# Optimization experiments

Measured on AMD Instinct MI355X. Metric: run time of the kernel, lower is better.

The kernel has to match this reference:

```python
import jax, jax.numpy as jnp
import numpy as np

LN_EPS = 1e-5


def setup_inputs() -> dict:
    key = jax.random.key(0)
    k1, k2 = jax.random.split(key, 2)
    B, C, D, H, W = 2, 96, 32, 128, 128
    out_dim = 2 * C
    x = jax.random.normal(k1, (B, C, D, H, W), dtype=jnp.float32)
    # nn.Linear(8*C, out_dim, bias=False): weight shape (out_dim, 8*C)
    w = jax.random.normal(k2, (out_dim, 8 * C), dtype=jnp.float32) * 0.02
    gamma = jnp.ones((8 * C,), dtype=jnp.float32)
    beta = jnp.zeros((8 * C,), dtype=jnp.float32)
    return {"x": x, "w": w, "gamma": gamma, "beta": beta}


def reference(x, w, gamma, beta):
    B, C, D, H, W = x.shape
    D2, H2, W2 = D // 2, H // 2, W // 2
    # Strided 2x2x2 gather: reshape then move (dd,hh,ww) offsets next to C.
    # torch.cat order [x0..x7] = (dd,hh,ww) lexicographic, dd most significant,
    # with C channels per block -> layout (..., dd, hh, ww, C) flattened.
    xr = x.reshape(B, C, D2, 2, H2, 2, W2, 2)
    xr = xr.transpose(0, 2, 4, 6, 3, 5, 7, 1)  # (B, D2, H2, W2, dd, hh, ww, C)
    xf = xr.reshape(B, D2, H2, W2, 8 * C)
    # LayerNorm over last dim
    mu = jnp.mean(xf, axis=-1, keepdims=True)
    xc = xf - mu
    var = jnp.mean(xc * xc, axis=-1, keepdims=True)
    xn = xc * jax.lax.rsqrt(var + LN_EPS) * gamma + beta
    # Linear (no bias): y = xn @ w.T
    y = jnp.einsum('bdhwc,oc->bdhwo', xn, w)
    # back to channels-first (B, out_dim, D2, H2, W2)
    return y.transpose(0, 4, 1, 2, 3)
```

## Files before the change

kernel.cpp:

```cpp
#include <hip/hip_runtime.h>
#include <hip/hip_bf16.h>

typedef __attribute__((ext_vector_type(8))) short short8;
typedef __attribute__((ext_vector_type(4))) float f32x4;

#define LN_EPS 1e-5f

__device__ __forceinline__ unsigned short f2bf(float f) {
  union { float f; unsigned u; } v; v.f = f;
  unsigned r = v.u + 0x7FFFu + ((v.u >> 16) & 1u);
  return (unsigned short)(r >> 16);
}

__device__ __forceinline__ int a_addr(int row, int colb) {
  return row * 1536 + (colb ^ ((row & 7) << 4));
}


__global__ __launch_bounds__(256) void pm_prep(
    const float* __restrict__ w, const float* __restrict__ g,
    const float* __restrict__ be, unsigned short* __restrict__ wg,
    float* __restrict__ sb) {
  const int o = blockIdx.x;
  const int t = threadIdx.x;
  const int lane = t & 63, wv = t >> 6;
  __shared__ float red[4][2];
  float sa = 0.f, ba = 0.f;
#pragma unroll
  for (int u = 0; u < 3; ++u) {
    int kp = t + 256 * u;
    int dh = kp / 192;
    int rem = kp - dh * 192;
    int c = rem >> 1, ww = rem & 1;
    int k = dh * 192 + ww * 96 + c;
    float wv_ = w[o * 768 + k];
    float v = wv_ * g[k];
    sa += v;
    ba += wv_ * be[k];
    int NT = o >> 4, ks = kp >> 5, qq = (kp >> 3) & 3, jj = kp & 7;
    wg[(((NT * 24 + ks) * 64) + qq * 16 + (o & 15)) * 8 + jj] = f2bf(v);
  }
#pragma unroll
  for (int d = 1; d < 64; d <<= 1) {
    sa += __shfl_xor(sa, d);
    ba += __shfl_xor(ba, d);
  }
  if (lane == 0) { red[wv][0] = sa; red[wv][1] = ba; }
  __syncthreads();
  if (t == 0) {
    sb[o] = red[0][0] + red[1][0] + red[2][0] + red[3][0];
    sb[192 + o] = red[0][1] + red[1][1] + red[2][1] + red[3][1];
  }
}

__global__ __launch_bounds__(256, 3) void pm_main(
    const float* __restrict__ x, const unsigned short* __restrict__ wg,
    const float* __restrict__ sb, float* __restrict__ out) {
  const int bid = blockIdx.x;
  const int wh = bid & 1;
  const int h2 = (bid >> 1) & 63;
  const int d2 = (bid >> 7) & 15;
  const int b = bid >> 11;
  const int t = threadIdx.x;
  const int lane = t & 63, wv = t >> 6;
  const int q = lane & 15, sc = lane >> 4;

  __shared__ __align__(16) unsigned char A_lds[32 * 1536];
  __shared__ float part[4][32][2];
  __shared__ float stats[32][2];

  const float* xb = x + (size_t)b * (96 * 32 * 128 * 128);
  const int cp0 = wv * 12 + sc * 3;
  const float* pc[3];
#pragma unroll
  for (int i = 0; i < 3; ++i)
    pc[i] = xb + (size_t)(2 * (cp0 + i)) * 524288 + wh * 64 + 4 * q;

  float sum0 = 0.f, sq0 = 0.f, sum1 = 0.f, sq1 = 0.f;
  float4 xa[2][3], xc[2][3];

  auto issue = [&](int p, int buf) {
    int off = (2 * d2 + (p >> 1)) * 16384 + (2 * h2 + (p & 1)) * 128;
#pragma unroll
    for (int i = 0; i < 3; ++i) {
      xa[buf][i] = *(const float4*)(pc[i] + off);
      xc[buf][i] = *(const float4*)(pc[i] + 524288 + off);
    }
  };

  auto consume = [&](int p, int buf) {
#pragma unroll
    for (int i = 0; i < 3; ++i) {
      float4 f0 = xa[buf][i], f1 = xc[buf][i];
      sum0 += (f0.x + f0.y) + (f1.x + f1.y);
      sq0  += f0.x * f0.x + f0.y * f0.y + f1.x * f1.x + f1.y * f1.y;
      sum1 += (f0.z + f0.w) + (f1.z + f1.w);
      sq1  += f0.z * f0.z + f0.w * f0.w + f1.z * f1.z + f1.w * f1.w;
      int colb = p * 384 + 8 * (cp0 + i);
      *(ushort4*)&A_lds[a_addr(2 * q, colb)] =
          make_ushort4(f2bf(f0.x), f2bf(f0.y), f2bf(f1.x), f2bf(f1.y));
      *(ushort4*)&A_lds[a_addr(2 * q + 1, colb)] =
          make_ushort4(f2bf(f0.z), f2bf(f0.w), f2bf(f1.z), f2bf(f1.w));
    }
  };

  const int al = lane & 15, ah = lane >> 4;
  const short8* wgs = (const short8*)wg;
  f32x4 acc[2][3];
#pragma unroll
  for (int mt = 0; mt < 2; ++mt)
#pragma unroll
    for (int nt = 0; nt < 3; ++nt) acc[mt][nt] = {0.f, 0.f, 0.f, 0.f};

  issue(0, 0);
  issue(1, 1);

#pragma unroll
  for (int p = 0; p < 4; ++p) {
    const int buf = p & 1;
    consume(p, buf);
    if (p == 3) {
      sum0 += __shfl_xor(sum0, 16); sum0 += __shfl_xor(sum0, 32);
      sq0  += __shfl_xor(sq0, 16);  sq0  += __shfl_xor(sq0, 32);
      sum1 += __shfl_xor(sum1, 16); sum1 += __shfl_xor(sum1, 32);
      sq1  += __shfl_xor(sq1, 16);  sq1  += __shfl_xor(sq1, 32);
      if (sc == 0) {
        part[wv][2 * q][0] = sum0;     part[wv][2 * q][1] = sq0;
        part[wv][2 * q + 1][0] = sum1; part[wv][2 * q + 1][1] = sq1;
      }
    }
    __syncthreads();

    short8 bfr[6][3];
#pragma unroll
    for (int ksi = 0; ksi < 6; ++ksi)
#pragma unroll
      for (int nt = 0; nt < 3; ++nt)
        bfr[ksi][nt] = wgs[((wv * 3 + nt) * 24 + (p * 6 + ksi)) * 64 + lane];

    if (p < 2) issue(p + 2, buf);

    if (p == 3) {
      int row = t & 31;
      float S = part[0][row][0] + part[1][row][0] + part[2][row][0] + part[3][row][0];
      float Q = part[0][row][1] + part[1][row][1] + part[2][row][1] + part[3][row][1];
      float mu = S * (1.f / 768.f);
      float var = Q * (1.f / 768.f) - mu * mu;
      float rs = rsqrtf(var + LN_EPS);
      stats[row][0] = rs;
      stats[row][1] = mu * rs;
    }

#pragma unroll
    for (int ksi = 0; ksi < 6; ++ksi) {
      int ks = p * 6 + ksi;
      short8 afr[2];
#pragma unroll
      for (int mt = 0; mt < 2; ++mt)
        afr[mt] = *(const short8*)&A_lds[a_addr(mt * 16 + al, ks * 64 + ah * 16)];
#pragma unroll
      for (int nt = 0; nt < 3; ++nt)
#pragma unroll
        for (int mt = 0; mt < 2; ++mt)
          acc[mt][nt] = __builtin_amdgcn_mfma_f32_16x16x32_bf16(afr[mt], bfr[ksi][nt], acc[mt][nt], 0, 0, 0);
    }
  }
  __syncthreads();

#pragma unroll
  for (int nt = 0; nt < 3; ++nt) {
    int o = wv * 48 + nt * 16 + al;
    float Sv = sb[o], Bv = sb[192 + o];
    float* ob = out + (((size_t)(b * 192 + o) * 16 + d2) * 64 + h2) * 64 + wh * 32;
#pragma unroll
    for (int mt = 0; mt < 2; ++mt) {
      int m0 = mt * 16 + ah * 4;
      float4 y;
      y.x = stats[m0 + 0][0] * acc[mt][nt][0] - stats[m0 + 0][1] * Sv + Bv;
      y.y = stats[m0 + 1][0] * acc[mt][nt][1] - stats[m0 + 1][1] * Sv + Bv;
      y.z = stats[m0 + 2][0] * acc[mt][nt][2] - stats[m0 + 2][1] * Sv + Bv;
      y.w = stats[m0 + 3][0] * acc[mt][nt][3] - stats[m0 + 3][1] * Sv + Bv;
      *(float4*)(ob + m0) = y;
    }
  }
}

extern "C" void kernel_launch(void* const* d_in, const int* in_sizes, int n_in,
                              void* d_out, int out_size, void* d_ws, size_t ws_size,
                              hipStream_t stream) {
  (void)in_sizes; (void)n_in; (void)out_size; (void)ws_size;
  const float* x  = (const float*)d_in[0];
  const float* w  = (const float*)d_in[1];
  const float* g  = (const float*)d_in[2];
  const float* be = (const float*)d_in[3];
  unsigned short* wg = (unsigned short*)d_ws;
  float* sb = (float*)((char*)d_ws + 192 * 768 * sizeof(unsigned short));
  pm_prep<<<192, 256, 0, stream>>>(w, g, be, wg, sb);
  pm_main<<<4096, 256, 0, stream>>>(x, wg, sb, (float*)d_out);
}
```

Measured before the change: 163.0 us.

## Make main kernel persistent over four tiles with cross-tile prefetch

Each block now processes four consecutive 32-row tiles instead of one, cutting the grid from 4096 to 1024 blocks. The prefetch pipeline is reduced to a single buffer but now crosses tile boundaries, so the next tile's first slice loads while the current epilogue and MFMA work run. This amortizes block launch and setup and keeps loads in flight between tiles. In exchange the grid is smaller, which may lower occupancy and load balance across CUs, and the prefetch depth drops from two stages to one.

```diff
diff --git a/kernel.cpp b/kernel.cpp
--- a/kernel.cpp
+++ b/kernel.cpp
@@ -57,10 +57,9 @@
     const float* __restrict__ x, const unsigned short* __restrict__ wg,
     const float* __restrict__ sb, float* __restrict__ out) {
   const int bid = blockIdx.x;
-  const int wh = bid & 1;
-  const int h2 = (bid >> 1) & 63;
-  const int d2 = (bid >> 7) & 15;
-  const int b = bid >> 11;
+  const int h2g = bid & 31;
+  const int d2 = (bid >> 5) & 15;
+  const int b = bid >> 9;
   const int t = threadIdx.x;
   const int lane = t & 63, wv = t >> 6;
   const int q = lane & 15, sc = lane >> 4;
@@ -74,24 +73,26 @@
   const float* pc[3];
 #pragma unroll
   for (int i = 0; i < 3; ++i)
-    pc[i] = xb + (size_t)(2 * (cp0 + i)) * 524288 + wh * 64 + 4 * q;
-
-  float sum0 = 0.f, sq0 = 0.f, sum1 = 0.f, sq1 = 0.f;
-  float4 xa[2][3], xc[2][3];
-
-  auto issue = [&](int p, int buf) {
-    int off = (2 * d2 + (p >> 1)) * 16384 + (2 * h2 + (p & 1)) * 128;
+    pc[i] = xb + (size_t)(2 * (cp0 + i)) * 524288 + 4 * q;
+
+  float sum0, sq0, sum1, sq1;
+  float4 xa[3], xc[3];
+
+  auto issue = [&](int tt, int p) {
+    int wh = tt & 1;
+    int h2 = 2 * h2g + (tt >> 1);
+    int off = (2 * d2 + (p >> 1)) * 16384 + (2 * h2 + (p & 1)) * 128 + wh * 64;
 #pragma unroll
     for (int i = 0; i < 3; ++i) {
-      xa[buf][i] = *(const float4*)(pc[i] + off);
-      xc[buf][i] = *(const float4*)(pc[i] + 524288 + off);
+      xa[i] = *(const float4*)(pc[i] + off);
+      xc[i] = *(const float4*)(pc[i] + 524288 + off);
     }
   };
 
-  auto consume = [&](int p, int buf) {
+  auto consume = [&](int p) {
 #pragma unroll
     for (int i = 0; i < 3; ++i) {
-      float4 f0 = xa[buf][i], f1 = xc[buf][i];
+      float4 f0 = xa[i], f1 = xc[i];
       sum0 += (f0.x + f0.y) + (f1.x + f1.y);
       sq0  += f0.x * f0.x + f0.y * f0.y + f1.x * f1.x + f1.y * f1.y;
       sum1 += (f0.z + f0.w) + (f1.z + f1.w);
@@ -106,81 +107,89 @@
 
   const int al = lane & 15, ah = lane >> 4;
   const short8* wgs = (const short8*)wg;
-  f32x4 acc[2][3];
-#pragma unroll
-  for (int mt = 0; mt < 2; ++mt)
-#pragma unroll
-    for (int nt = 0; nt < 3; ++nt) acc[mt][nt] = {0.f, 0.f, 0.f, 0.f};
 
   issue(0, 0);
-  issue(1, 1);
-
-#pragma unroll
-  for (int p = 0; p < 4; ++p) {
-    const int buf = p & 1;
-    consume(p, buf);
-    if (p == 3) {
-      sum0 += __shfl_xor(sum0, 16); sum0 += __shfl_xor(sum0, 32);
-      sq0  += __shfl_xor(sq0, 16);  sq0  += __shfl_xor(sq0, 32);
-      sum1 += __shfl_xor(sum1, 16); sum1 += __shfl_xor(sum1, 32);
-      sq1  += __shfl_xor(sq1, 16);  sq1  += __shfl_xor(sq1, 32);
-      if (sc == 0) {
-        part[wv][2 * q][0] = sum0;     part[wv][2 * q][1] = sq0;
-        part[wv][2 * q + 1][0] = sum1; part[wv][2 * q + 1][1] = sq1;
+
+#pragma unroll 1
+  for (int tt = 0; tt < 4; ++tt) {
+    f32x4 acc[2][3];
+#pragma unroll
+    for (int mt = 0; mt < 2; ++mt)
+#pragma unroll
+      for (int nt = 0; nt < 3; ++nt) acc[mt][nt] = {0.f, 0.f, 0.f, 0.f};
+    sum0 = 0.f; sq0 = 0.f; sum1 = 0.f; sq1 = 0.f;
+
+#pragma unroll
+    for (int p = 0; p < 4; ++p) {
+      consume(p);
+      if (p == 3) {
+        sum0 += __shfl_xor(sum0, 16); sum0 += __shfl_xor(sum0, 32);
+        sq0  += __shfl_xor(sq0, 16);  sq0  += __shfl_xor(sq0, 32);
+        sum1 += __shfl_xor(sum1, 16); sum1 += __shfl_xor(sum1, 32);
+        sq1  += __shfl_xor(sq1, 16);  sq1  += __shfl_xor(sq1, 32);
+        if (sc == 0) {
+          part[wv][2 * q][0] = sum0;     part[wv][2 * q][1] = sq0;
+          part[wv][2 * q + 1][0] = sum1; part[wv][2 * q + 1][1] = sq1;
+        }
+      }
+      __syncthreads();
+
+      short8 bfr[6][3];
+#pragma unroll
+      for (int ksi = 0; ksi < 6; ++ksi)
+#pragma unroll
+        for (int nt = 0; nt < 3; ++nt)
+          bfr[ksi][nt] = wgs[((wv * 3 + nt) * 24 + (p * 6 + ksi)) * 64 + lane];
+
+      if (p < 3) issue(tt, p + 1);
+      else if (tt < 3) issue(tt + 1, 0);
+
+      if (p == 3) {
+        int row = t & 31;
+        float S = part[0][row][0] + part[1][row][0] + part[2][row][0] + part[3][row][0];
+        float Q = part[0][row][1] + part[1][row][1] + part[2][row][1] + part[3][row][1];
+        float mu = S * (1.f / 768.f);
+        float var = Q * (1.f / 768.f) - mu * mu;
+        float rs = rsqrtf(var + LN_EPS);
+        stats[row][0] = rs;
+        stats[row][1] = mu * rs;
+      }
+
+#pragma unroll
+      for (int ksi = 0; ksi < 6; ++ksi) {
+        int ks = p * 6 + ksi;
+        short8 afr[2];
+#pragma unroll
+        for (int mt = 0; mt < 2; ++mt)
+          afr[mt] = *(const short8*)&A_lds[a_addr(mt * 16 + al, ks * 64 + ah * 16)];
+#pragma unroll
+        for (int nt = 0; nt < 3; ++nt)
+#pragma unroll
+          for (int mt = 0; mt < 2; ++mt)
+            acc[mt][nt] = __builtin_amdgcn_mfma_f32_16x16x32_bf16(afr[mt], bfr[ksi][nt], acc[mt][nt], 0, 0, 0);
       }
     }
     __syncthreads();
 
-    short8 bfr[6][3];
-#pragma unroll
-    for (int ksi = 0; ksi < 6; ++ksi)
-#pragma unroll
-      for (int nt = 0; nt < 3; ++nt)
-        bfr[ksi][nt] = wgs[((wv * 3 + nt) * 24 + (p * 6 + ksi)) * 64 + lane];
-
-    if (p < 2) issue(p + 2, buf);
-
-    if (p == 3) {
-      int row = t & 31;
-      float S = part[0][row][0] + part[1][row][0] + part[2][row][0] + part[3][row][0];
-      float Q = part[0][row][1] + part[1][row][1] + part[2][row][1] + part[3][row][1];
-      float mu = S * (1.f / 768.f);
-      float var = Q * (1.f / 768.f) - mu * mu;
-      float rs = rsqrtf(var + LN_EPS);
-      stats[row][0] = rs;
-      stats[row][1] = mu * rs;
-    }
-
-#pragma unroll
-    for (int ksi = 0; ksi < 6; ++ksi) {
-      int ks = p * 6 + ksi;
-      short8 afr[2];
-#pragma unroll
-      for (int mt = 0; mt < 2; ++mt)
-        afr[mt] = *(const short8*)&A_lds[a_addr(mt * 16 + al, ks * 64 + ah * 16)];
-#pragma unroll
-      for (int nt = 0; nt < 3; ++nt)
-#pragma unroll
-        for (int mt = 0; mt < 2; ++mt)
-          acc[mt][nt] = __builtin_amdgcn_mfma_f32_16x16x32_bf16(afr[mt], bfr[ksi][nt], acc[mt][nt], 0, 0, 0);
-    }
-  }
-  __syncthreads();
-
-#pragma unroll
-  for (int nt = 0; nt < 3; ++nt) {
-    int o = wv * 48 + nt * 16 + al;
-    float Sv = sb[o], Bv = sb[192 + o];
-    float* ob = out + (((size_t)(b * 192 + o) * 16 + d2) * 64 + h2) * 64 + wh * 32;
-#pragma unroll
-    for (int mt = 0; mt < 2; ++mt) {
-      int m0 = mt * 16 + ah * 4;
-      float4 y;
-      y.x = stats[m0 + 0][0] * acc[mt][nt][0] - stats[m0 + 0][1] * Sv + Bv;
-      y.y = stats[m0 + 1][0] * acc[mt][nt][1] - stats[m0 + 1][1] * Sv + Bv;
-      y.z = stats[m0 + 2][0] * acc[mt][nt][2] - stats[m0 + 2][1] * Sv + Bv;
-      y.w = stats[m0 + 3][0] * acc[mt][nt][3] - stats[m0 + 3][1] * Sv + Bv;
-      *(float4*)(ob + m0) = y;
+    {
+      int wh = tt & 1;
+      int h2 = 2 * h2g + (tt >> 1);
+#pragma unroll
+      for (int nt = 0; nt < 3; ++nt) {
+        int o = wv * 48 + nt * 16 + al;
+        float Sv = sb[o], Bv = sb[192 + o];
+        float* ob = out + (((size_t)(b * 192 + o) * 16 + d2) * 64 + h2) * 64 + wh * 32;
+#pragma unroll
+        for (int mt = 0; mt < 2; ++mt) {
+          int m0 = mt * 16 + ah * 4;
+          float4 y;
+          y.x = stats[m0 + 0][0] * acc[mt][nt][0] - stats[m0 + 0][1] * Sv + Bv;
+          y.y = stats[m0 + 1][0] * acc[mt][nt][1] - stats[m0 + 1][1] * Sv + Bv;
+          y.z = stats[m0 + 2][0] * acc[mt][nt][2] - stats[m0 + 2][1] * Sv + Bv;
+          y.w = stats[m0 + 3][0] * acc[mt][nt][3] - stats[m0 + 3][1] * Sv + Bv;
+          *(float4*)(ob + m0) = y;
+        }
+      }
     }
   }
 }
@@ -196,5 +205,5 @@
   unsigned short* wg = (unsigned short*)d_ws;
   float* sb = (float*)((char*)d_ws + 192 * 768 * sizeof(unsigned short));
   pm_prep<<<192, 256, 0, stream>>>(w, g, be, wg, sb);
-  pm_main<<<4096, 256, 0, stream>>>(x, wg, sb, (float*)d_out);
-}
+  pm_main<<<1024, 256, 0, stream>>>(x, wg, sb, (float*)d_out);
+}
```

Measured after the change: 560.6 us. 3.44x slower.
